# Kernel tuning notes

Hardware: AMD Instinct MI355X
Metric: run time of the kernel (lower is better)

The kernel has to match this reference:

```python
import jax, jax.numpy as jnp
import numpy as np

B, D, H = 64, 2048, 2048


def setup_inputs() -> dict:
    key = jax.random.key(0)
    ks = jax.random.split(key, 10)
    s = 1.0 / np.sqrt(D)  # Linear init scale
    # small z scale keeps exp() gates in a sane range
    return {
        "t": jnp.zeros((), jnp.float32),
        "z": jax.random.normal(ks[0], (B, D), jnp.float32) * 0.02,
        "K": jax.random.normal(ks[1], (B, D), jnp.float32) * 0.02,
        "V": jax.random.normal(ks[2], (B, D, D), jnp.float32) * 0.02,
        "Wq": jax.random.normal(ks[3], (D, D), jnp.float32) * s,
        "bq": jnp.zeros((D,), jnp.float32),
        "Wk": jax.random.normal(ks[4], (D, D), jnp.float32) * s,
        "bk": jnp.zeros((D,), jnp.float32),
        "Wv": jax.random.normal(ks[5], (D, D), jnp.float32) * s,
        "bv": jnp.zeros((D,), jnp.float32),
        "W1": jax.random.normal(ks[6], (D, H), jnp.float32) * s,
        "b1": jnp.zeros((H,), jnp.float32),
        "W2": jax.random.normal(ks[7], (H, D), jnp.float32) * (1.0 / np.sqrt(H)),
        "b2": jnp.zeros((D,), jnp.float32),
    }


def reference(t, z, K, V, Wq, bq, Wk, bk, Wv, bv, W1, b1, W2, b2):
    # get_ode_gradient_nn: 2-layer tanh MLP (stand-in for user ode_func_net)
    dz = jnp.tanh(z @ W1 + b1) @ W2 + b2                 # [B, D]
    dK = jnp.exp(z @ Wk + bk)                            # exp gate, [B, D]
    v = z @ Wv + bv                                      # [B, D]
    dV = jnp.einsum("bd,be->bde", v, dK)                # rank-1 outer update, [B, D, D]
    q = jnp.exp(z @ Wq + bq)                             # [B, D]
    a = jnp.sum(q * dK, axis=-1, keepdims=True)          # q . dK, [B, 1]
    dq = q * (dz @ Wq + bq)                              # [B, D]
    da = a + jnp.sum(dq * K, axis=-1, keepdims=True)     # [B, 1]
    dc = jnp.einsum("bde,be->bd", dV, q) + jnp.einsum("bde,be->bd", V, dq)  # [B, D]
    return (dz, da, dc, dK, dV)
```

## Files before the change

kernel.cpp:

```cpp
#include <hip/hip_runtime.h>
#include <cstddef>
#include <math.h>

#define BB 64
#define DD 2048
#define HH 2048
#define BD (BB*DD)
#define WN (2048*2048)

typedef unsigned short u16;
typedef __attribute__((ext_vector_type(8))) short bf16x8;
typedef __attribute__((ext_vector_type(4))) float f32x4;
typedef __attribute__((ext_vector_type(4))) float f4;

__device__ __forceinline__ u16 f2b(float x) {
    union { float f; unsigned u; } v; v.f = x;
    unsigned r = v.u + 0x7FFFu + ((v.u >> 16) & 1u);
    return (u16)(r >> 16);
}

__device__ __forceinline__ void gload16(const void* g, void* l) {
    __builtin_amdgcn_global_load_lds(
        (__attribute__((address_space(1))) void*)g,
        (__attribute__((address_space(3))) void*)l, 16, 0, 0);
}


__global__ __launch_bounds__(256) void wconv(
    const float* __restrict__ W0, const float* __restrict__ W1,
    const float* __restrict__ W2, const float* __restrict__ W3,
    const float* __restrict__ W4, u16* __restrict__ wt,
    const float* __restrict__ z, u16* __restrict__ zb)
{
    int t = threadIdx.x;
    if (blockIdx.z == 5) {
        if (blockIdx.y != 0 || blockIdx.x >= 32) return;
        int i0 = blockIdx.x * 4096 + t * 16;
        u16 o[16];
#pragma unroll
        for (int q = 0; q < 4; ++q) {
            float4 f = *(const float4*)&z[i0 + q * 4];
            o[q*4+0] = f2b(f.x); o[q*4+1] = f2b(f.y);
            o[q*4+2] = f2b(f.z); o[q*4+3] = f2b(f.w);
        }
        *(bf16x8*)&zb[i0]     = *(bf16x8*)&o[0];
        *(bf16x8*)&zb[i0 + 8] = *(bf16x8*)&o[8];
        return;
    }
    const float* W;
    switch (blockIdx.z) {
        case 0: W = W0; break; case 1: W = W1; break;
        case 2: W = W2; break; case 3: W = W3; break;
        default: W = W4; break;
    }
    u16* T = wt + (size_t)blockIdx.z * WN;

    __shared__ u16 tile[64][66];
    int k0 = blockIdx.x * 64, n0 = blockIdx.y * 64;
    {
        int r = t >> 2, c0 = (t & 3) * 16;
        const float* src = W + (size_t)(k0 + r) * DD + n0 + c0;
#pragma unroll
        for (int q = 0; q < 4; ++q) {
            float4 f = *(const float4*)(src + q * 4);
            tile[r][c0 + q*4 + 0] = f2b(f.x);
            tile[r][c0 + q*4 + 1] = f2b(f.y);
            tile[r][c0 + q*4 + 2] = f2b(f.z);
            tile[r][c0 + q*4 + 3] = f2b(f.w);
        }
    }
    __syncthreads();
    {
        int rn = t >> 2, ck = (t & 3) * 16;
        u16 o[16];
#pragma unroll
        for (int j = 0; j < 16; ++j) o[j] = tile[ck + j][rn];
        u16* dst = T + (size_t)(n0 + rn) * DD + k0 + ck;
        *(bf16x8*)dst       = *(bf16x8*)&o[0];
        *(bf16x8*)(dst + 8) = *(bf16x8*)&o[8];
    }
}

__device__ __forceinline__ void gemm_bf16_body(
    const u16* __restrict__ A, const u16* __restrict__ Wt,
    float* __restrict__ P, int kc)
{
    __shared__ u16 Als[64 * 32];
    __shared__ u16 Wls[64 * 32];
    const int t = threadIdx.x, w = t >> 6, lane = t & 63;
    const int n0 = blockIdx.x * 64;
    const int k0 = blockIdx.y * kc;

    f32x4 acc[4];
#pragma unroll
    for (int mt = 0; mt < 4; ++mt) acc[mt] = (f32x4){0.f, 0.f, 0.f, 0.f};

    const int srow = lane >> 2;
    const int sk   = (lane & 3) * 8;
    const u16* gA = A  + (size_t)(w * 16 + srow) * DD + k0 + sk;
    const u16* gW = Wt + (size_t)(n0 + w * 16 + srow) * DD + k0 + sk;
    u16* lA = &Als[w * 512];
    u16* lW = &Wls[w * 512];

    const int lane15 = lane & 15;
    const int k8 = (lane >> 4) * 8;

    for (int kk = 0; kk < kc; kk += 32) {
        gload16(gA, lA);
        gload16(gW, lW);
        gA += 32; gW += 32;
        __syncthreads();

        bf16x8 bfrag = *(const bf16x8*)&Wls[(w * 16 + lane15) * 32 + k8];
#pragma unroll
        for (int mt = 0; mt < 4; ++mt) {
            bf16x8 afrag = *(const bf16x8*)&Als[(mt * 16 + lane15) * 32 + k8];
            acc[mt] = __builtin_amdgcn_mfma_f32_16x16x32_bf16(
                afrag, bfrag, acc[mt], 0, 0, 0);
        }
        __syncthreads();
    }

    const int col = n0 + w * 16 + lane15;
    const int r4 = (lane >> 4) * 4;
#pragma unroll
    for (int mt = 0; mt < 4; ++mt)
#pragma unroll
        for (int j = 0; j < 4; ++j)
            P[(size_t)(mt * 16 + r4 + j) * DD + col] = acc[mt][j];
}

__global__ __launch_bounds__(256) void gemm_bf16_single(
    const u16* __restrict__ A, const u16* __restrict__ Wt,
    float* __restrict__ part, int kc)
{
    float* P = part + (size_t)blockIdx.y * 64 * DD;
    gemm_bf16_body(A, Wt, P, kc);
}

__global__ __launch_bounds__(256) void gemm_bf16_kv(
    const u16* __restrict__ A, const u16* __restrict__ Wkt,
    const u16* __restrict__ Wvt, float* __restrict__ p0,
    float* __restrict__ p1, int kc)
{
    const u16* Wt = blockIdx.z ? Wvt : Wkt;
    float* P = (blockIdx.z ? p1 : p0) + (size_t)blockIdx.y * 64 * DD;
    gemm_bf16_body(A, Wt, P, kc);
}

__global__ __launch_bounds__(256) void gemm_bf16_q(
    const u16* __restrict__ zb, const u16* __restrict__ dzb,
    const u16* __restrict__ Wqt, float* __restrict__ part, int kc)
{
    const u16* A = blockIdx.z ? dzb : zb;
    float* P = part + ((size_t)blockIdx.y * 128 + blockIdx.z * 64) * DD;
    gemm_bf16_body(A, Wqt, P, kc);
}

__global__ __launch_bounds__(256) void ep_h(
    const float* __restrict__ p, const float* __restrict__ b1,
    u16* __restrict__ hb, int KS)
{
    int i = blockIdx.x * 256 + threadIdx.x;
    float s = b1[i & (DD - 1)];
    for (int ks = 0; ks < KS; ++ks) s += p[(size_t)ks * BD + i];
    hb[i] = f2b(tanhf(s));
}

__global__ __launch_bounds__(256) void ep_dz(
    const float* __restrict__ p, const float* __restrict__ b2,
    float* __restrict__ dz, u16* __restrict__ dzb, int KS)
{
    int i = blockIdx.x * 256 + threadIdx.x;
    float s = b2[i & (DD - 1)];
    for (int ks = 0; ks < KS; ++ks) s += p[(size_t)ks * BD + i];
    dz[i]  = s;
    dzb[i] = f2b(s);
}

__global__ __launch_bounds__(256) void ep_kv(
    const float* __restrict__ pk, const float* __restrict__ pv,
    const float* __restrict__ bk, const float* __restrict__ bv,
    float* __restrict__ dKo, float* __restrict__ vo, int KS)
{
    int i = blockIdx.x * 256 + threadIdx.x;
    int d = i & (DD - 1);
    float sk = 0.f, sv = 0.f;
    for (int ks = 0; ks < KS; ++ks) {
        sk += pk[(size_t)ks * BD + i];
        sv += pv[(size_t)ks * BD + i];
    }
    dKo[i] = expf(sk + bk[d]);
    vo[i]  = sv + bv[d];
}

__global__ __launch_bounds__(256) void ep_q_dq(
    const float* __restrict__ pq, const float* __restrict__ bq,
    float* __restrict__ qo, float* __restrict__ dqo, int KS)
{
    int i = blockIdx.x * 256 + threadIdx.x;
    int b = i >> 11, d = i & (DD - 1);
    float sq = 0.f, sd = 0.f;
    for (int ks = 0; ks < KS; ++ks) {
        const float* P = pq + (size_t)ks * (128 * DD);
        sq += P[(size_t)b * DD + d];
        sd += P[(size_t)(b + 64) * DD + d];
    }
    float bb = bq[d];
    float qv = expf(sq + bb);
    qo[i]  = qv;
    dqo[i] = qv * (sd + bb);
}

template<int MT>
__device__ __forceinline__ void gemm_body_f32(
    const float* __restrict__ A0, const float* __restrict__ A1,
    const float* __restrict__ W, float* __restrict__ part, int kc)
{
    constexpr int KC = 32;
    constexpr int RT = MT / 16;
    __shared__ float As[KC][MT];
    __shared__ float Ws[KC][64];

    const int t  = threadIdx.x;
    const int n0 = blockIdx.x * 64;
    const int k0 = blockIdx.y * kc;
    const int i  = t >> 4;
    const int j  = t & 15;

    float acc[RT][4];
#pragma unroll
    for (int r = 0; r < RT; ++r)
#pragma unroll
        for (int c = 0; c < 4; ++c) acc[r][c] = 0.f;

    for (int kk0 = 0; kk0 < kc; kk0 += KC) {
        {
            int kk = t >> 3;
            int nn = (t & 7) << 3;
            const float* s = W + (size_t)(k0 + kk0 + kk) * DD + n0 + nn;
            *(float4*)&Ws[kk][nn]     = *(const float4*)s;
            *(float4*)&Ws[kk][nn + 4] = *(const float4*)(s + 4);
        }
        if constexpr (MT == 64) {
            int m  = t & 63;
            int kb = (t >> 6) << 3;
            const float* s = A0 + (size_t)m * DD + k0 + kk0 + kb;
            float4 a0 = *(const float4*)s;
            float4 a1 = *(const float4*)(s + 4);
            As[kb+0][m] = a0.x; As[kb+1][m] = a0.y;
            As[kb+2][m] = a0.z; As[kb+3][m] = a0.w;
            As[kb+4][m] = a1.x; As[kb+5][m] = a1.y;
            As[kb+6][m] = a1.z; As[kb+7][m] = a1.w;
        } else {
            int m  = t & 127;
            int kb = (t >> 7) << 4;
            const float* base = (m < 64) ? (A0 + (size_t)m * DD)
                                         : (A1 + (size_t)(m - 64) * DD);
            const float* s = base + k0 + kk0 + kb;
#pragma unroll
            for (int p = 0; p < 4; ++p) {
                float4 av = *(const float4*)(s + p * 4);
                As[kb+p*4+0][m] = av.x; As[kb+p*4+1][m] = av.y;
                As[kb+p*4+2][m] = av.z; As[kb+p*4+3][m] = av.w;
            }
        }
        __syncthreads();
#pragma unroll
        for (int kk = 0; kk < KC; ++kk) {
            float4 wv = *(float4*)&Ws[kk][j << 2];
#pragma unroll
            for (int rq = 0; rq < RT / 4; ++rq) {
                float4 av = *(float4*)&As[kk][i * RT + rq * 4];
                acc[rq*4+0][0] = fmaf(av.x, wv.x, acc[rq*4+0][0]);
                acc[rq*4+0][1] = fmaf(av.x, wv.y, acc[rq*4+0][1]);
                acc[rq*4+0][2] = fmaf(av.x, wv.z, acc[rq*4+0][2]);
                acc[rq*4+0][3] = fmaf(av.x, wv.w, acc[rq*4+0][3]);
                acc[rq*4+1][0] = fmaf(av.y, wv.x, acc[rq*4+1][0]);
                acc[rq*4+1][1] = fmaf(av.y, wv.y, acc[rq*4+1][1]);
                acc[rq*4+1][2] = fmaf(av.y, wv.z, acc[rq*4+1][2]);
                acc[rq*4+1][3] = fmaf(av.y, wv.w, acc[rq*4+1][3]);
                acc[rq*4+2][0] = fmaf(av.z, wv.x, acc[rq*4+2][0]);
                acc[rq*4+2][1] = fmaf(av.z, wv.y, acc[rq*4+2][1]);
                acc[rq*4+2][2] = fmaf(av.z, wv.z, acc[rq*4+2][2]);
                acc[rq*4+2][3] = fmaf(av.z, wv.w, acc[rq*4+2][3]);
                acc[rq*4+3][0] = fmaf(av.w, wv.x, acc[rq*4+3][0]);
                acc[rq*4+3][1] = fmaf(av.w, wv.y, acc[rq*4+3][1]);
                acc[rq*4+3][2] = fmaf(av.w, wv.z, acc[rq*4+3][2]);
                acc[rq*4+3][3] = fmaf(av.w, wv.w, acc[rq*4+3][3]);
            }
        }
        __syncthreads();
    }

    float* P = part + (size_t)blockIdx.y * MT * DD + n0 + (j << 2);
#pragma unroll
    for (int r = 0; r < RT; ++r)
        *(float4*)&P[(size_t)(i * RT + r) * DD] =
            make_float4(acc[r][0], acc[r][1], acc[r][2], acc[r][3]);
}

__global__ __launch_bounds__(256) void gemm64(
    const float* __restrict__ A, const float* __restrict__ W,
    float* __restrict__ part, int kc)
{ gemm_body_f32<64>(A, A, W, part, kc); }

__global__ __launch_bounds__(256) void gemm64_z2(
    const float* __restrict__ A,
    const float* __restrict__ W0, const float* __restrict__ W1,
    float* __restrict__ p0, float* __restrict__ p1, int kc)
{
    const float* W = blockIdx.z ? W1 : W0;
    float*       P = blockIdx.z ? p1 : p0;
    gemm_body_f32<64>(A, A, W, P, kc);
}

__global__ __launch_bounds__(256) void gemm128(
    const float* __restrict__ A0, const float* __restrict__ A1,
    const float* __restrict__ W, float* __restrict__ part, int kc)
{ gemm_body_f32<128>(A0, A1, W, part, kc); }

__global__ __launch_bounds__(256) void epilogue_f32(
    const float* __restrict__ part, const float* __restrict__ bias,
    float* __restrict__ out, int act, int KS)
{
    int i = blockIdx.x * 256 + threadIdx.x;
    float s = bias[i & (DD - 1)];
    for (int ks = 0; ks < KS; ++ks) s += part[(size_t)ks * BD + i];
    if (act == 1) s = tanhf(s);
    out[i] = s;
}

__global__ __launch_bounds__(256) void reduce_a_da(
    const float* __restrict__ q, const float* __restrict__ dK,
    const float* __restrict__ dq, const float* __restrict__ Kin,
    float* __restrict__ a_ws, float* __restrict__ da_out)
{
    int b = blockIdx.x;
    int t = threadIdx.x;
    const float* qb  = q   + (size_t)b * DD;
    const float* dKb = dK  + (size_t)b * DD;
    const float* dqb = dq  + (size_t)b * DD;
    const float* Kb  = Kin + (size_t)b * DD;

    float s1 = 0.f, s2 = 0.f;
    for (int i = t; i < DD; i += 256) {
        s1 = fmaf(qb[i],  dKb[i], s1);
        s2 = fmaf(dqb[i], Kb[i],  s2);
    }
#pragma unroll
    for (int off = 32; off; off >>= 1) {
        s1 += __shfl_down(s1, off);
        s2 += __shfl_down(s2, off);
    }
    __shared__ float r1[4], r2[4];
    if ((t & 63) == 0) { r1[t >> 6] = s1; r2[t >> 6] = s2; }
    __syncthreads();
    if (t == 0) {
        float a  = r1[0] + r1[1] + r1[2] + r1[3];
        float k2 = r2[0] + r2[1] + r2[2] + r2[3];
        a_ws[b]   = a;
        da_out[b] = a + k2;
    }
}

__global__ __launch_bounds__(256) void dv_write(
    const float* __restrict__ v, const float* __restrict__ dK,
    float* __restrict__ dV)
{
    int b     = blockIdx.x >> 5;
    int chunk = blockIdx.x & 31;
    int wave  = threadIdx.x >> 6;
    int lane  = threadIdx.x & 63;

    const f4* dK4 = (const f4*)(dK + ((size_t)b << 11));
    f4 dKr[8];
#pragma unroll
    for (int u = 0; u < 8; ++u) dKr[u] = dK4[u * 64 + lane];

    int row0 = chunk * 64 + wave * 16;
    for (int rr = 0; rr < 16; ++rr) {
        int row = row0 + rr;
        float vr = v[((size_t)b << 11) + row];
        f4* dV4 = (f4*)(dV + (((size_t)((b << 11) | row)) << 11));
#pragma unroll
        for (int u = 0; u < 8; ++u) {
            f4 o = vr * dKr[u];
            __builtin_nontemporal_store(o, &dV4[u * 64 + lane]);
        }
    }
}

__global__ __launch_bounds__(256) void dc_dot(
    const float* __restrict__ V, const float* __restrict__ v,
    const float* __restrict__ dq, const float* __restrict__ a,
    float* __restrict__ dc)
{
    int b     = blockIdx.x >> 5;
    int chunk = blockIdx.x & 31;
    int wave  = threadIdx.x >> 6;
    int lane  = threadIdx.x & 63;

    const f4* dq4 = (const f4*)(dq + ((size_t)b << 11));
    f4 dqr[8];
#pragma unroll
    for (int u = 0; u < 8; ++u) dqr[u] = dq4[u * 64 + lane];
    float ab = a[b];

    int row0 = chunk * 64 + wave * 16;
    for (int g = 0; g < 4; ++g) {
        float dot[4];
#pragma unroll
        for (int r2 = 0; r2 < 4; ++r2) {
            int row = row0 + g * 4 + r2;
            const f4* V4 = (const f4*)(V + (((size_t)((b << 11) | row)) << 11));
            float d = 0.f;
#pragma unroll
            for (int u = 0; u < 8; ++u) {
                f4 Vv = __builtin_nontemporal_load(&V4[u * 64 + lane]);
                d += Vv[0] * dqr[u][0] + Vv[1] * dqr[u][1]
                   + Vv[2] * dqr[u][2] + Vv[3] * dqr[u][3];
            }
            dot[r2] = d;
        }
#pragma unroll
        for (int r2 = 0; r2 < 4; ++r2) {
            float d = dot[r2];
#pragma unroll
            for (int s = 32; s; s >>= 1) d += __shfl_down(d, s);
            if (lane == 0) {
                int row = row0 + g * 4 + r2;
                dc[((size_t)b << 11) + row] =
                    v[((size_t)b << 11) + row] * ab + d;
            }
        }
    }
}

extern "C" void kernel_launch(void* const* d_in, const int* in_sizes, int n_in,
                              void* d_out, int out_size, void* d_ws, size_t ws_size,
                              hipStream_t stream)
{
    const float* z   = (const float*)d_in[1];
    const float* Kin = (const float*)d_in[2];
    const float* Vin = (const float*)d_in[3];
    const float* Wq  = (const float*)d_in[4];
    const float* bq  = (const float*)d_in[5];
    const float* Wk  = (const float*)d_in[6];
    const float* bk  = (const float*)d_in[7];
    const float* Wv  = (const float*)d_in[8];
    const float* bv  = (const float*)d_in[9];
    const float* W1  = (const float*)d_in[10];
    const float* b1  = (const float*)d_in[11];
    const float* W2  = (const float*)d_in[12];
    const float* b2  = (const float*)d_in[13];

    float* out   = (float*)d_out;
    float* o_dz  = out;
    float* o_da  = out + BD;
    float* o_dc  = out + BD + BB;
    float* o_dK  = out + 2 * BD + BB;
    float* o_dV  = out + 3 * BD + BB;

    float* ws    = (float*)d_ws;
    float* ws_v  = ws;
    float* ws_q  = ws + BD;
    float* ws_dq = ws + 2 * BD;
    float* ws_a  = ws + 3 * BD;
    float* ws_h  = ws + 3 * BD + 64;
    u16*   zb    = (u16*)(ws + 4 * BD + 64);
    u16*   hb    = zb + BD;
    u16*   dzb   = hb + BD;
    u16*   wt    = dzb + BD;
    float* poolb = (float*)(wt + 5ull * WN);

    const size_t pre_fl = 4ull * BD + 64 + (3ull * BD + 5ull * WN) / 2;

    int KS = 0;
    for (int ks = 16; ks >= 4; ks >>= 1)
        if ((pre_fl + 2ull * ks * BD) * 4ull <= ws_size) { KS = ks; break; }

    dim3 blk(256);
    dim3 gE(BD / 256);

    if (KS) {
        int kc = DD / KS;
        float* p0 = poolb;
        float* p1 = poolb + (size_t)KS * BD;

        dim3 gW(32, 32, 6);
        dim3 gG(32, KS);
        dim3 gG2(32, KS, 2);

        wconv<<<gW, blk, 0, stream>>>(W1, W2, Wk, Wv, Wq, wt, z, zb);

        u16* W1t = wt;
        u16* W2t = wt + 1ull * WN;
        u16* Wkt = wt + 2ull * WN;
        u16* Wvt = wt + 3ull * WN;
        u16* Wqt = wt + 4ull * WN;

        gemm_bf16_single<<<gG, blk, 0, stream>>>(zb, W1t, p0, kc);
        ep_h<<<gE, blk, 0, stream>>>(p0, b1, hb, KS);

        gemm_bf16_single<<<gG, blk, 0, stream>>>(hb, W2t, p0, kc);
        ep_dz<<<gE, blk, 0, stream>>>(p0, b2, o_dz, dzb, KS);

        gemm_bf16_kv<<<gG2, blk, 0, stream>>>(zb, Wkt, Wvt, p0, p1, kc);
        ep_kv<<<gE, blk, 0, stream>>>(p0, p1, bk, bv, o_dK, ws_v, KS);

        dv_write<<<dim3(BB * 32), blk, 0, stream>>>(ws_v, o_dK, o_dV);

        gemm_bf16_q<<<gG2, blk, 0, stream>>>(zb, dzb, Wqt, p0, kc);
        ep_q_dq<<<gE, blk, 0, stream>>>(p0, bq, ws_q, ws_dq, KS);
    } else {
        float* pool = ws + 4 * BD + 64;
        int KSf = 16;
        while (KSf > 1 &&
               ((size_t)(4 * BD + 64) + 2ull * KSf * BD) * 4ull > ws_size)
            KSf >>= 1;
        int kc = DD / KSf;
        float* p0 = pool;
        float* p1 = pool + (size_t)KSf * BD;

        dim3 gG(DD / 64, KSf);
        dim3 gG2(DD / 64, KSf, 2);

        gemm64<<<gG, blk, 0, stream>>>(z, W1, p0, kc);
        epilogue_f32<<<gE, blk, 0, stream>>>(p0, b1, ws_h, 1, KSf);

        gemm64<<<gG, blk, 0, stream>>>(ws_h, W2, p0, kc);
        epilogue_f32<<<gE, blk, 0, stream>>>(p0, b2, o_dz, 0, KSf);

        gemm64_z2<<<gG2, blk, 0, stream>>>(z, Wk, Wv, p0, p1, kc);
        ep_kv<<<gE, blk, 0, stream>>>(p0, p1, bk, bv, o_dK, ws_v, KSf);

        dv_write<<<dim3(BB * 32), blk, 0, stream>>>(ws_v, o_dK, o_dV);

        gemm128<<<gG, blk, 0, stream>>>(z, o_dz, Wq, p0, kc);
        ep_q_dq<<<gE, blk, 0, stream>>>(p0, bq, ws_q, ws_dq, KSf);
    }

    reduce_a_da<<<dim3(BB), blk, 0, stream>>>(ws_q, o_dK, ws_dq, Kin, ws_a, o_da);

    dc_dot<<<dim3(BB * 32), blk, 0, stream>>>(Vin, ws_v, ws_dq, ws_a, o_dc);
}
```

Baseline: 445.7 us.

## Merge GEMMs, weight conversion and dV writes into fewer heterogeneous launches

Restructures the bf16 path so that independent work shares launches. The W1/Wk/Wv GEMMs run alongside the W2/Wq weight conversion in one kernel, and the h and kv epilogues are fused into one launch. The dV outer-product stores are split across the W2 GEMM and Wq GEMM kernels so the memory-bound writes overlap compute-bound MFMA work. This removes several launches and fills idle CUs, but it needs a third partial-sum pool (a larger workspace requirement that may force a smaller KS) and mixes block types with different resource use.

```diff
diff --git a/kernel.cpp b/kernel.cpp
--- a/kernel.cpp
+++ b/kernel.cpp
@@ -26,47 +26,22 @@
 }
 
 
-__global__ __launch_bounds__(256) void wconv(
-    const float* __restrict__ W0, const float* __restrict__ W1,
-    const float* __restrict__ W2, const float* __restrict__ W3,
-    const float* __restrict__ W4, u16* __restrict__ wt,
-    const float* __restrict__ z, u16* __restrict__ zb)
+__device__ __forceinline__ void wconv_tile(
+    u16* sm, const float* __restrict__ W, u16* __restrict__ T,
+    int kb, int nb)
 {
     int t = threadIdx.x;
-    if (blockIdx.z == 5) {
-        if (blockIdx.y != 0 || blockIdx.x >= 32) return;
-        int i0 = blockIdx.x * 4096 + t * 16;
-        u16 o[16];
-#pragma unroll
-        for (int q = 0; q < 4; ++q) {
-            float4 f = *(const float4*)&z[i0 + q * 4];
-            o[q*4+0] = f2b(f.x); o[q*4+1] = f2b(f.y);
-            o[q*4+2] = f2b(f.z); o[q*4+3] = f2b(f.w);
-        }
-        *(bf16x8*)&zb[i0]     = *(bf16x8*)&o[0];
-        *(bf16x8*)&zb[i0 + 8] = *(bf16x8*)&o[8];
-        return;
-    }
-    const float* W;
-    switch (blockIdx.z) {
-        case 0: W = W0; break; case 1: W = W1; break;
-        case 2: W = W2; break; case 3: W = W3; break;
-        default: W = W4; break;
-    }
-    u16* T = wt + (size_t)blockIdx.z * WN;
-
-    __shared__ u16 tile[64][66];
-    int k0 = blockIdx.x * 64, n0 = blockIdx.y * 64;
+    int k0 = kb * 64, n0 = nb * 64;
     {
         int r = t >> 2, c0 = (t & 3) * 16;
         const float* src = W + (size_t)(k0 + r) * DD + n0 + c0;
 #pragma unroll
         for (int q = 0; q < 4; ++q) {
             float4 f = *(const float4*)(src + q * 4);
-            tile[r][c0 + q*4 + 0] = f2b(f.x);
-            tile[r][c0 + q*4 + 1] = f2b(f.y);
-            tile[r][c0 + q*4 + 2] = f2b(f.z);
-            tile[r][c0 + q*4 + 3] = f2b(f.w);
+            sm[r * 66 + c0 + q*4 + 0] = f2b(f.x);
+            sm[r * 66 + c0 + q*4 + 1] = f2b(f.y);
+            sm[r * 66 + c0 + q*4 + 2] = f2b(f.z);
+            sm[r * 66 + c0 + q*4 + 3] = f2b(f.w);
         }
     }
     __syncthreads();
@@ -74,7 +49,7 @@
         int rn = t >> 2, ck = (t & 3) * 16;
         u16 o[16];
 #pragma unroll
-        for (int j = 0; j < 16; ++j) o[j] = tile[ck + j][rn];
+        for (int j = 0; j < 16; ++j) o[j] = sm[(ck + j) * 66 + rn];
         u16* dst = T + (size_t)(n0 + rn) * DD + k0 + ck;
         *(bf16x8*)dst       = *(bf16x8*)&o[0];
         *(bf16x8*)(dst + 8) = *(bf16x8*)&o[8];
@@ -82,14 +57,14 @@
 }
 
 __device__ __forceinline__ void gemm_bf16_body(
-    const u16* __restrict__ A, const u16* __restrict__ Wt,
-    float* __restrict__ P, int kc)
-{
-    __shared__ u16 Als[64 * 32];
-    __shared__ u16 Wls[64 * 32];
+    u16* sm, const u16* __restrict__ A, const u16* __restrict__ Wt,
+    float* __restrict__ P, int kc, int nblk, int kblk)
+{
+    u16* Als = sm;
+    u16* Wls = sm + 2048;
     const int t = threadIdx.x, w = t >> 6, lane = t & 63;
-    const int n0 = blockIdx.x * 64;
-    const int k0 = blockIdx.y * kc;
+    const int n0 = nblk * 64;
+    const int k0 = kblk * kc;
 
     f32x4 acc[4];
 #pragma unroll
@@ -130,41 +105,126 @@
             P[(size_t)(mt * 16 + r4 + j) * DD + col] = acc[mt][j];
 }
 
-__global__ __launch_bounds__(256) void gemm_bf16_single(
-    const u16* __restrict__ A, const u16* __restrict__ Wt,
-    float* __restrict__ part, int kc)
-{
-    float* P = part + (size_t)blockIdx.y * 64 * DD;
-    gemm_bf16_body(A, Wt, P, kc);
-}
-
-__global__ __launch_bounds__(256) void gemm_bf16_kv(
-    const u16* __restrict__ A, const u16* __restrict__ Wkt,
-    const u16* __restrict__ Wvt, float* __restrict__ p0,
-    float* __restrict__ p1, int kc)
-{
-    const u16* Wt = blockIdx.z ? Wvt : Wkt;
-    float* P = (blockIdx.z ? p1 : p0) + (size_t)blockIdx.y * 64 * DD;
-    gemm_bf16_body(A, Wt, P, kc);
-}
-
-__global__ __launch_bounds__(256) void gemm_bf16_q(
-    const u16* __restrict__ zb, const u16* __restrict__ dzb,
-    const u16* __restrict__ Wqt, float* __restrict__ part, int kc)
-{
-    const u16* A = blockIdx.z ? dzb : zb;
-    float* P = part + ((size_t)blockIdx.y * 128 + blockIdx.z * 64) * DD;
-    gemm_bf16_body(A, Wqt, P, kc);
-}
-
-__global__ __launch_bounds__(256) void ep_h(
-    const float* __restrict__ p, const float* __restrict__ b1,
-    u16* __restrict__ hb, int KS)
-{
-    int i = blockIdx.x * 256 + threadIdx.x;
-    float s = b1[i & (DD - 1)];
-    for (int ks = 0; ks < KS; ++ks) s += p[(size_t)ks * BD + i];
-    hb[i] = f2b(tanhf(s));
+__device__ __forceinline__ void dv_body(
+    const float* __restrict__ v, const float* __restrict__ dK,
+    float* __restrict__ dV, int b, int chunk)
+{
+    int wave = threadIdx.x >> 6;
+    int lane = threadIdx.x & 63;
+
+    const f4* dK4 = (const f4*)(dK + ((size_t)b << 11));
+    f4 dKr[8];
+#pragma unroll
+    for (int u = 0; u < 8; ++u) dKr[u] = dK4[u * 64 + lane];
+
+    int row0 = chunk * 64 + wave * 16;
+    for (int rr = 0; rr < 16; ++rr) {
+        int row = row0 + rr;
+        float vr = v[((size_t)b << 11) + row];
+        f4* dV4 = (f4*)(dV + (((size_t)((b << 11) | row)) << 11));
+#pragma unroll
+        for (int u = 0; u < 8; ++u) {
+            f4 o = vr * dKr[u];
+            __builtin_nontemporal_store(o, &dV4[u * 64 + lane]);
+        }
+    }
+}
+
+
+__global__ __launch_bounds__(256) void wconv1(
+    const float* __restrict__ W1, const float* __restrict__ Wk,
+    const float* __restrict__ Wv, u16* __restrict__ W1t,
+    u16* __restrict__ Wkt, u16* __restrict__ Wvt,
+    const float* __restrict__ z, u16* __restrict__ zb)
+{
+    __shared__ u16 sm[64 * 66];
+    int t = threadIdx.x;
+    if (blockIdx.z == 3) {
+        if (blockIdx.y != 0 || blockIdx.x >= 32) return;
+        int i0 = blockIdx.x * 4096 + t * 16;
+        u16 o[16];
+#pragma unroll
+        for (int q = 0; q < 4; ++q) {
+            float4 f = *(const float4*)&z[i0 + q * 4];
+            o[q*4+0] = f2b(f.x); o[q*4+1] = f2b(f.y);
+            o[q*4+2] = f2b(f.z); o[q*4+3] = f2b(f.w);
+        }
+        *(bf16x8*)&zb[i0]     = *(bf16x8*)&o[0];
+        *(bf16x8*)&zb[i0 + 8] = *(bf16x8*)&o[8];
+        return;
+    }
+    const float* W = (blockIdx.z == 0) ? W1 : (blockIdx.z == 1) ? Wk : Wv;
+    u16* T = (blockIdx.z == 0) ? W1t : (blockIdx.z == 1) ? Wkt : Wvt;
+    wconv_tile(sm, W, T, blockIdx.x, blockIdx.y);
+}
+
+__global__ __launch_bounds__(256) void mA(
+    const u16* __restrict__ zb, const u16* __restrict__ W1t,
+    const u16* __restrict__ Wkt, const u16* __restrict__ Wvt,
+    float* __restrict__ ph, float* __restrict__ pk, float* __restrict__ pv,
+    const float* __restrict__ W2, const float* __restrict__ Wq,
+    u16* __restrict__ W2t, u16* __restrict__ Wqt, int kc, int nG)
+{
+    __shared__ u16 sm[64 * 66];
+    int blk = blockIdx.x;
+    if (blk < 3 * nG) {
+        int sel = blk / nG;
+        int r   = blk - sel * nG;
+        const u16* Wt = (sel == 0) ? W1t : (sel == 1) ? Wkt : Wvt;
+        float* pool   = (sel == 0) ? ph  : (sel == 1) ? pk  : pv;
+        int nblk = r & 31, kblk = r >> 5;
+        gemm_bf16_body(sm, zb, Wt, pool + (size_t)kblk * 64 * DD,
+                       kc, nblk, kblk);
+    } else {
+        int r = blk - 3 * nG;
+        const float* W = (r < 1024) ? W2 : Wq;
+        u16* T         = (r < 1024) ? W2t : Wqt;
+        int rr = r & 1023;
+        wconv_tile(sm, W, T, rr & 31, rr >> 5);
+    }
+}
+
+__global__ __launch_bounds__(256) void mEp(
+    const float* __restrict__ ph, const float* __restrict__ pk,
+    const float* __restrict__ pv, const float* __restrict__ b1,
+    const float* __restrict__ bk, const float* __restrict__ bv,
+    u16* __restrict__ hb, float* __restrict__ dKo, float* __restrict__ vo,
+    int KS)
+{
+    int blk = blockIdx.x;
+    if (blk < 512) {
+        int i = blk * 256 + threadIdx.x;
+        float s = b1[i & (DD - 1)];
+        for (int ks = 0; ks < KS; ++ks) s += ph[(size_t)ks * BD + i];
+        hb[i] = f2b(tanhf(s));
+    } else {
+        int i = (blk - 512) * 256 + threadIdx.x;
+        int d = i & (DD - 1);
+        float sk = 0.f, sv = 0.f;
+        for (int ks = 0; ks < KS; ++ks) {
+            sk += pk[(size_t)ks * BD + i];
+            sv += pv[(size_t)ks * BD + i];
+        }
+        dKo[i] = expf(sk + bk[d]);
+        vo[i]  = sv + bv[d];
+    }
+}
+
+__global__ __launch_bounds__(256) void mDZ(
+    const float* __restrict__ v, const float* __restrict__ dK,
+    float* __restrict__ dV, const u16* __restrict__ hb,
+    const u16* __restrict__ W2t, float* __restrict__ p0, int kc, int nG)
+{
+    __shared__ u16 sm[4096];
+    int blk = blockIdx.x;
+    if (blk < 1024) {
+        dv_body(v, dK, dV, blk >> 5, blk & 31);
+    } else {
+        int r = blk - 1024;
+        int nblk = r & 31, kblk = r >> 5;
+        gemm_bf16_body(sm, hb, W2t, p0 + (size_t)kblk * 64 * DD,
+                       kc, nblk, kblk);
+    }
 }
 
 __global__ __launch_bounds__(256) void ep_dz(
@@ -178,20 +238,26 @@
     dzb[i] = f2b(s);
 }
 
-__global__ __launch_bounds__(256) void ep_kv(
-    const float* __restrict__ pk, const float* __restrict__ pv,
-    const float* __restrict__ bk, const float* __restrict__ bv,
-    float* __restrict__ dKo, float* __restrict__ vo, int KS)
-{
-    int i = blockIdx.x * 256 + threadIdx.x;
-    int d = i & (DD - 1);
-    float sk = 0.f, sv = 0.f;
-    for (int ks = 0; ks < KS; ++ks) {
-        sk += pk[(size_t)ks * BD + i];
-        sv += pv[(size_t)ks * BD + i];
-    }
-    dKo[i] = expf(sk + bk[d]);
-    vo[i]  = sv + bv[d];
+__global__ __launch_bounds__(256) void mQ(
+    const float* __restrict__ v, const float* __restrict__ dK,
+    float* __restrict__ dV, const u16* __restrict__ zb,
+    const u16* __restrict__ dzb, const u16* __restrict__ Wqt,
+    float* __restrict__ pq, int kc, int nG)
+{
+    __shared__ u16 sm[4096];
+    int blk = blockIdx.x;
+    if (blk < 1024) {
+        dv_body(v, dK, dV, 32 + (blk >> 5), blk & 31);
+    } else {
+        int r = blk - 1024;
+        int zsel = (r >= nG) ? 1 : 0;
+        int rr = r - zsel * nG;
+        int nblk = rr & 31, kblk = rr >> 5;
+        const u16* A = zsel ? dzb : zb;
+        gemm_bf16_body(sm, A, Wqt,
+                       pq + ((size_t)kblk * 128 + zsel * 64) * DD,
+                       kc, nblk, kblk);
+    }
 }
 
 __global__ __launch_bounds__(256) void ep_q_dq(
@@ -331,6 +397,29 @@
     out[i] = s;
 }
 
+__global__ __launch_bounds__(256) void ep_kv_f32(
+    const float* __restrict__ pk, const float* __restrict__ pv,
+    const float* __restrict__ bk, const float* __restrict__ bv,
+    float* __restrict__ dKo, float* __restrict__ vo, int KS)
+{
+    int i = blockIdx.x * 256 + threadIdx.x;
+    int d = i & (DD - 1);
+    float sk = 0.f, sv = 0.f;
+    for (int ks = 0; ks < KS; ++ks) {
+        sk += pk[(size_t)ks * BD + i];
+        sv += pv[(size_t)ks * BD + i];
+    }
+    dKo[i] = expf(sk + bk[d]);
+    vo[i]  = sv + bv[d];
+}
+
+__global__ __launch_bounds__(256) void dv_write_full(
+    const float* __restrict__ v, const float* __restrict__ dK,
+    float* __restrict__ dV)
+{
+    dv_body(v, dK, dV, blockIdx.x >> 5, blockIdx.x & 31);
+}
+
 __global__ __launch_bounds__(256) void reduce_a_da(
     const float* __restrict__ q, const float* __restrict__ dK,
     const float* __restrict__ dq, const float* __restrict__ Kin,
@@ -361,33 +450,6 @@
         float k2 = r2[0] + r2[1] + r2[2] + r2[3];
         a_ws[b]   = a;
         da_out[b] = a + k2;
-    }
-}
-
-__global__ __launch_bounds__(256) void dv_write(
-    const float* __restrict__ v, const float* __restrict__ dK,
-    float* __restrict__ dV)
-{
-    int b     = blockIdx.x >> 5;
-    int chunk = blockIdx.x & 31;
-    int wave  = threadIdx.x >> 6;
-    int lane  = threadIdx.x & 63;
-
-    const f4* dK4 = (const f4*)(dK + ((size_t)b << 11));
-    f4 dKr[8];
-#pragma unroll
-    for (int u = 0; u < 8; ++u) dKr[u] = dK4[u * 64 + lane];
-
-    int row0 = chunk * 64 + wave * 16;
-    for (int rr = 0; rr < 16; ++rr) {
-        int row = row0 + rr;
-        float vr = v[((size_t)b << 11) + row];
-        f4* dV4 = (f4*)(dV + (((size_t)((b << 11) | row)) << 11));
-#pragma unroll
-        for (int u = 0; u < 8; ++u) {
-            f4 o = vr * dKr[u];
-            __builtin_nontemporal_store(o, &dV4[u * 64 + lane]);
-        }
     }
 }
 
@@ -478,21 +540,19 @@
 
     int KS = 0;
     for (int ks = 16; ks >= 4; ks >>= 1)
-        if ((pre_fl + 2ull * ks * BD) * 4ull <= ws_size) { KS = ks; break; }
+        if ((pre_fl + 3ull * ks * BD) * 4ull <= ws_size) { KS = ks; break; }
 
     dim3 blk(256);
     dim3 gE(BD / 256);
 
     if (KS) {
         int kc = DD / KS;
+        int nG = 32 * KS;
+        float* ph = poolb;
+        float* pk = poolb + (size_t)KS * BD;
+        float* pv = poolb + 2ull * KS * BD;
         float* p0 = poolb;
-        float* p1 = poolb + (size_t)KS * BD;
-
-        dim3 gW(32, 32, 6);
-        dim3 gG(32, KS);
-        dim3 gG2(32, KS, 2);
-
-        wconv<<<gW, blk, 0, stream>>>(W1, W2, Wk, Wv, Wq, wt, z, zb);
+        float* pq = poolb;
 
         u16* W1t = wt;
         u16* W2t = wt + 1ull * WN;
@@ -500,19 +560,24 @@
         u16* Wvt = wt + 3ull * WN;
         u16* Wqt = wt + 4ull * WN;
 
-        gemm_bf16_single<<<gG, blk, 0, stream>>>(zb, W1t, p0, kc);
-        ep_h<<<gE, blk, 0, stream>>>(p0, b1, hb, KS);
-
-        gemm_bf16_single<<<gG, blk, 0, stream>>>(hb, W2t, p0, kc);
+        wconv1<<<dim3(32, 32, 4), blk, 0, stream>>>(
+            W1, Wk, Wv, W1t, Wkt, Wvt, z, zb);
+
+        mA<<<dim3(3 * nG + 2048), blk, 0, stream>>>(
+            zb, W1t, Wkt, Wvt, ph, pk, pv, W2, Wq, W2t, Wqt, kc, nG);
+
+        mEp<<<dim3(1024), blk, 0, stream>>>(
+            ph, pk, pv, b1, bk, bv, hb, o_dK, ws_v, KS);
+
+        mDZ<<<dim3(1024 + nG), blk, 0, stream>>>(
+            ws_v, o_dK, o_dV, hb, W2t, p0, kc, nG);
+
         ep_dz<<<gE, blk, 0, stream>>>(p0, b2, o_dz, dzb, KS);
 
-        gemm_bf16_kv<<<gG2, blk, 0, stream>>>(zb, Wkt, Wvt, p0, p1, kc);
-        ep_kv<<<gE, blk, 0, stream>>>(p0, p1, bk, bv, o_dK, ws_v, KS);
-
-        dv_write<<<dim3(BB * 32), blk, 0, stream>>>(ws_v, o_dK, o_dV);
-
-        gemm_bf16_q<<<gG2, blk, 0, stream>>>(zb, dzb, Wqt, p0, kc);
-        ep_q_dq<<<gE, blk, 0, stream>>>(p0, bq, ws_q, ws_dq, KS);
+        mQ<<<dim3(1024 + 2 * nG), blk, 0, stream>>>(
+            ws_v, o_dK, o_dV, zb, dzb, Wqt, pq, kc, nG);
+
+        ep_q_dq<<<gE, blk, 0, stream>>>(pq, bq, ws_q, ws_dq, KS);
     } else {
         float* pool = ws + 4 * BD + 64;
         int KSf = 16;
@@ -533,9 +598,9 @@
         epilogue_f32<<<gE, blk, 0, stream>>>(p0, b2, o_dz, 0, KSf);
 
         gemm64_z2<<<gG2, blk, 0, stream>>>(z, Wk, Wv, p0, p1, kc);
-        ep_kv<<<gE, blk, 0, stream>>>(p0, p1, bk, bv, o_dK, ws_v, KSf);
-
-        dv_write<<<dim3(BB * 32), blk, 0, stream>>>(ws_v, o_dK, o_dV);
+        ep_kv_f32<<<gE, blk, 0, stream>>>(p0, p1, bk, bv, o_dK, ws_v, KSf);
+
+        dv_write_full<<<dim3(BB * 32), blk, 0, stream>>>(ws_v, o_dK, o_dV);
 
         gemm128<<<gG, blk, 0, stream>>>(z, o_dz, Wq, p0, kc);
         ep_q_dq<<<gE, blk, 0, stream>>>(p0, bq, ws_q, ws_dq, KSf);
```

Result: faster. 425.6 us (-4.5%).
